# Performance work log

Hardware: AMD Instinct MI355X
Metric: run time of the kernel (lower is better)

The kernel has to match this reference:

```python
import jax, jax.numpy as jnp
import numpy as np

D_MODEL = 768
NUM_HEADS = 12
HEAD_DIM = D_MODEL // NUM_HEADS
B, T = 2, 4096


def setup_inputs() -> dict:
    key = jax.random.key(0)
    k1, k2, k3, k4, k5 = jax.random.split(key, 5)
    s_in = 1.0 / np.sqrt(D_MODEL)
    return {
        "x": jax.random.normal(k1, (B, T, D_MODEL), dtype=jnp.float32),
        "w_qkv": jax.random.normal(k2, (3 * D_MODEL, D_MODEL), dtype=jnp.float32) * s_in,
        "b_qkv": jax.random.normal(k3, (3 * D_MODEL,), dtype=jnp.float32) * 0.01,
        "w_out": jax.random.normal(k4, (D_MODEL, D_MODEL), dtype=jnp.float32) * s_in,
        "b_out": jax.random.normal(k5, (D_MODEL,), dtype=jnp.float32) * 0.01,
    }


def reference(x, w_qkv, b_qkv, w_out, b_out):
    b, t, c = x.shape
    # qkv: [B,T,3C] -> [3,B,H,T,Dh]  (torch Linear: x @ W.T + b)
    qkv = (x @ w_qkv.T + b_qkv).reshape(b, t, 3, NUM_HEADS, HEAD_DIM)
    qkv = jnp.transpose(qkv, (2, 0, 3, 1, 4))
    q, k, v = qkv[0], qkv[1], qkv[2]
    scale = 1.0 / np.sqrt(HEAD_DIM)
    scores = jnp.einsum("bhqd,bhkd->bhqk", q, k) * scale  # [B,H,T,T]
    causal = jnp.tril(jnp.ones((t, t), dtype=bool))
    scores = jnp.where(causal, scores, -jnp.inf)
    weights = jax.nn.softmax(scores, axis=-1)
    out = jnp.einsum("bhqk,bhkd->bhqd", weights, v)  # [B,H,T,Dh]
    out = jnp.transpose(out, (0, 2, 1, 3)).reshape(b, t, c)
    return out @ w_out.T + b_out
```

## Files before the change

kernel.cpp:

```cpp
#include <hip/hip_runtime.h>


#define NHEADS 12
#define DHEAD  64
#define TSEQ   4096
#define BATCH  2
#define CMODEL 768
#define MTOT   (BATCH * TSEQ)
#define NQKV   (3 * CMODEL)
#define NBH    (BATCH * NHEADS)

typedef __attribute__((ext_vector_type(8))) short s16x8;
typedef __attribute__((ext_vector_type(4))) float f32x4;
typedef __attribute__((ext_vector_type(4))) unsigned short u16x4;
typedef __attribute__((ext_vector_type(2))) unsigned int u32x2;

__device__ __forceinline__ unsigned short f2bf(float f) {
    unsigned u = __builtin_bit_cast(unsigned, f);
    u += 0x7fffu + ((u >> 16) & 1u);
    return (unsigned short)(u >> 16);
}

__device__ __forceinline__ unsigned pk2bf(float a, float b) {
    return (unsigned)f2bf(a) | ((unsigned)f2bf(b) << 16);
}

__device__ __forceinline__ unsigned cvtpk(float lo, float hi) {
    unsigned r;
    asm("v_cvt_pk_bf16_f32 %0, %1, %2" : "=v"(r) : "v"(lo), "v"(hi));
    return r;
}

__device__ __forceinline__ float fexp2(float x) {
    return __builtin_amdgcn_exp2f(x);
}

__device__ __forceinline__ void async_load16(const void* g, void* l) {
    __builtin_amdgcn_global_load_lds(
        (const __attribute__((address_space(1))) unsigned*)g,
        (__attribute__((address_space(3))) unsigned*)l, 16, 0, 0);
}

__device__ __forceinline__ void raw_barrier() {
    __builtin_amdgcn_sched_barrier(0);
    __builtin_amdgcn_s_barrier();
    __builtin_amdgcn_sched_barrier(0);
}

__global__ __launch_bounds__(256) void cvt3_kernel(
    const float* __restrict__ s0, const float* __restrict__ s1,
    const float* __restrict__ s2,
    unsigned short* __restrict__ d0, unsigned short* __restrict__ d1,
    unsigned short* __restrict__ d2, int n0, int n1, int n2)
{
    int i = blockIdx.x * 256 + threadIdx.x;
    const float* s; unsigned short* d; int j;
    if (i < n0)                { s = s0; d = d0; j = i; }
    else if (i < n0 + n1)      { s = s1; d = d1; j = i - n0; }
    else if (i < n0 + n1 + n2) { s = s2; d = d2; j = i - n0 - n1; }
    else return;
    f32x4 v = ((const f32x4*)s)[j];
    u32x2 o;
    o.x = pk2bf(v.x, v.y);
    o.y = pk2bf(v.z, v.w);
    ((u32x2*)d)[j] = o;
}

__global__ __launch_bounds__(256) void gemm_qkv_kernel(
    const unsigned short* __restrict__ A,
    const unsigned short* __restrict__ Bw,
    const float* __restrict__ bias,
    unsigned short* __restrict__ Qb,
    unsigned short* __restrict__ Kb,
    unsigned short* __restrict__ Vt)
{
    __shared__ unsigned short sA[128][64];
    __shared__ unsigned short sB[128][64];
    const int idx = blockIdx.x + blockIdx.y * 18;
    const int lid = (idx & 7) * 144 + (idx >> 3);
    const int n0 = (lid % 18) * 128;
    const int m0 = (lid / 18) * 128;
    const int tid = threadIdx.x;
    const int l = tid & 63, g = l >> 4, l15 = l & 15;
    const int w = tid >> 6, wm = w & 1, wn = w >> 1;
    const int wbase = tid & 192;
    const int seg = n0 / 768;

    f32x4 acc[4][4];
#pragma unroll
    for (int a = 0; a < 4; a++)
#pragma unroll
        for (int b = 0; b < 4; b++) acc[a][b] = (f32x4){0.f, 0.f, 0.f, 0.f};

    if (seg < 2) {
        for (int k0 = 0; k0 < 768; k0 += 64) {
#pragma unroll
            for (int i = 0; i < 4; i++) {
                const int idx2 = i * 256 + tid;
                const int row = idx2 >> 3, pc = idx2 & 7;
                const int lc = pc ^ (row & 7);
                async_load16(&A[(size_t)(m0 + row) * 768 + k0 + lc * 8],
                             &sA[0][0] + (size_t)(i * 256 + wbase) * 8);
                async_load16(&Bw[(size_t)(n0 + row) * 768 + k0 + lc * 8],
                             &sB[0][0] + (size_t)(i * 256 + wbase) * 8);
            }
            __syncthreads();
#pragma unroll
            for (int ks = 0; ks < 2; ks++) {
                const int cc = ((ks * 4 + g) ^ (l15 & 7)) * 8;
                s16x8 af[4], bf[4];
#pragma unroll
                for (int mt = 0; mt < 4; mt++)
                    af[mt] = *(const s16x8*)&sA[wm * 64 + mt * 16 + l15][cc];
#pragma unroll
                for (int nt = 0; nt < 4; nt++)
                    bf[nt] = *(const s16x8*)&sB[wn * 64 + nt * 16 + l15][cc];
#pragma unroll
                for (int nt = 0; nt < 4; nt++)
#pragma unroll
                    for (int mt = 0; mt < 4; mt++)
                        acc[nt][mt] = __builtin_amdgcn_mfma_f32_16x16x32_bf16(
                            bf[nt], af[mt], acc[nt][mt], 0, 0, 0);
            }
            __syncthreads();
        }

        unsigned short* dst = (seg == 0) ? Qb : Kb;
        const float sc = (seg == 0) ? 0.18033688011f : 1.0f;
        const int hh = ((n0 - seg * 768) + wn * 64) >> 6;
#pragma unroll
        for (int nt = 0; nt < 4; nt++) {
            const int dh = nt * 16 + g * 4;
            const f32x4 bv4 = *(const f32x4*)&bias[n0 + wn * 64 + dh];
#pragma unroll
            for (int mt = 0; mt < 4; mt++) {
                const int m = m0 + wm * 64 + mt * 16 + l15;
                const int b = m >> 12, t = m & 4095;
                u32x2 pk;
                pk.x = pk2bf((acc[nt][mt][0] + bv4[0]) * sc,
                             (acc[nt][mt][1] + bv4[1]) * sc);
                pk.y = pk2bf((acc[nt][mt][2] + bv4[2]) * sc,
                             (acc[nt][mt][3] + bv4[3]) * sc);
                *(u32x2*)&dst[(((size_t)(b * NHEADS + hh) * TSEQ + t) << 6) + dh] = pk;
            }
        }
    } else {
        for (int k0 = 0; k0 < 768; k0 += 64) {
#pragma unroll
            for (int i = 0; i < 4; i++) {
                const int idx2 = i * 256 + tid;
                const int row = idx2 >> 3, pc = idx2 & 7;
                const int lc = pc ^ (row & 7);
                async_load16(&A[(size_t)(m0 + row) * 768 + k0 + lc * 8],
                             &sA[0][0] + (size_t)(i * 256 + wbase) * 8);
                async_load16(&Bw[(size_t)(n0 + row) * 768 + k0 + lc * 8],
                             &sB[0][0] + (size_t)(i * 256 + wbase) * 8);
            }
            __syncthreads();
#pragma unroll
            for (int ks = 0; ks < 2; ks++) {
                const int cc = ((ks * 4 + g) ^ (l15 & 7)) * 8;
                s16x8 af[4], bf[4];
#pragma unroll
                for (int mt = 0; mt < 4; mt++)
                    af[mt] = *(const s16x8*)&sA[wm * 64 + mt * 16 + l15][cc];
#pragma unroll
                for (int nt = 0; nt < 4; nt++)
                    bf[nt] = *(const s16x8*)&sB[wn * 64 + nt * 16 + l15][cc];
#pragma unroll
                for (int mt = 0; mt < 4; mt++)
#pragma unroll
                    for (int nt = 0; nt < 4; nt++)
                        acc[mt][nt] = __builtin_amdgcn_mfma_f32_16x16x32_bf16(
                            af[mt], bf[nt], acc[mt][nt], 0, 0, 0);
            }
            __syncthreads();
        }

#pragma unroll
        for (int nt = 0; nt < 4; nt++) {
            const int n = n0 + wn * 64 + nt * 16 + l15;
            const float bv = bias[n];
            const int hh = (n - 1536) >> 6;
            const int dh = n & 63;
#pragma unroll
            for (int mt = 0; mt < 4; mt++) {
                const int mg = m0 + wm * 64 + mt * 16 + g * 4;
                const int b = mg >> 12, t = mg & 4095;
                u32x2 pk;
                pk.x = pk2bf(acc[mt][nt][0] + bv, acc[mt][nt][1] + bv);
                pk.y = pk2bf(acc[mt][nt][2] + bv, acc[mt][nt][3] + bv);
                *(u32x2*)&Vt[((size_t)(b * NHEADS + hh) * DHEAD + dh) * TSEQ + t] = pk;
            }
        }
    }
}

__device__ __forceinline__ void process_tile(
    const unsigned short (&sKb)[64][64],
    const unsigned short (&sVb)[64][64],
    unsigned short (&sPTw)[2][16][64],
    const s16x8 (&qa)[2][2],
    f32x4 (&o)[2][4], f32x4 (&lac)[2],
    s16x8 vones, int kt, int qg0, bool mask, int g, int l15)
{
    const int xk = l15 & 7;
    const int qg1 = qg0 + 16;

    f32x4 st[2][4];
#pragma unroll
    for (int nt = 0; nt < 4; nt++) {
        st[0][nt] = (f32x4){0.f, 0.f, 0.f, 0.f};
        st[1][nt] = (f32x4){0.f, 0.f, 0.f, 0.f};
    }
    __builtin_amdgcn_s_setprio(1);
#pragma unroll
    for (int ks = 0; ks < 2; ks++) {
        const int cc = ((ks * 4 + g) ^ xk) * 8;
#pragma unroll
        for (int nt = 0; nt < 4; nt++) {
            const s16x8 akf = *(const s16x8*)&sKb[nt * 16 + l15][cc];
            st[0][nt] = __builtin_amdgcn_mfma_f32_16x16x32_bf16(
                akf, qa[0][ks], st[0][nt], 0, 0, 0);
            st[1][nt] = __builtin_amdgcn_mfma_f32_16x16x32_bf16(
                akf, qa[1][ks], st[1][nt], 0, 0, 0);
        }
    }
    __builtin_amdgcn_s_setprio(0);

    if (mask) {
#pragma unroll
        for (int nt = 0; nt < 4; nt++)
#pragma unroll
            for (int r = 0; r < 4; r++) {
                const int key = kt + nt * 16 + g * 4 + r;
                if (key > qg0) st[0][nt][r] = -1e30f;
                if (key > qg1) st[1][nt][r] = -1e30f;
            }
    }

#pragma unroll
    for (int qf = 0; qf < 2; qf++) {
#pragma unroll
        for (int nt = 0; nt < 4; nt++) {
            float p0 = fexp2(st[qf][nt][0]);
            float p1 = fexp2(st[qf][nt][1]);
            float p2 = fexp2(st[qf][nt][2]);
            float p3 = fexp2(st[qf][nt][3]);
            u32x2 pk;
            pk.x = cvtpk(p0, p1);
            pk.y = cvtpk(p2, p3);
            const int phys = ((nt * 2 + (g >> 1)) ^ xk) * 8 + (g & 1) * 4;
            *(u32x2*)&sPTw[qf][l15][phys] = pk;
        }
    }

    __builtin_amdgcn_s_setprio(1);
#pragma unroll
    for (int ks = 0; ks < 2; ks++) {
        const int cc = ((ks * 4 + g) ^ xk) * 8;
        const s16x8 bp0 = *(const s16x8*)&sPTw[0][l15][cc];
        const s16x8 bp1 = *(const s16x8*)&sPTw[1][l15][cc];
#pragma unroll
        for (int nt = 0; nt < 4; nt++) {
            const s16x8 avf = *(const s16x8*)&sVb[nt * 16 + l15][cc];
            o[0][nt] = __builtin_amdgcn_mfma_f32_16x16x32_bf16(
                avf, bp0, o[0][nt], 0, 0, 0);
            o[1][nt] = __builtin_amdgcn_mfma_f32_16x16x32_bf16(
                avf, bp1, o[1][nt], 0, 0, 0);
        }
        lac[0] = __builtin_amdgcn_mfma_f32_16x16x32_bf16(vones, bp0, lac[0], 0, 0, 0);
        lac[1] = __builtin_amdgcn_mfma_f32_16x16x32_bf16(vones, bp1, lac[1], 0, 0, 0);
    }
    __builtin_amdgcn_s_setprio(0);
}

__global__ __launch_bounds__(256, 3) void attn_kernel(
    const unsigned short* __restrict__ Qb,
    const unsigned short* __restrict__ Kb,
    const unsigned short* __restrict__ Vt,
    unsigned short* __restrict__ Ob,
    float* __restrict__ oPart,
    float* __restrict__ lPart)
{
    __shared__ unsigned short sK[2][64][64];
    __shared__ unsigned short sV[2][64][64];
    __shared__ unsigned short sPT[4][2][16][64];
    const int bh   = blockIdx.x;
    const int p    = blockIdx.y >> 1;
    const int half = blockIdx.y & 1;
    const int jA = p, jB = 31 - p;
    const int nA = 2 * p + 2;
    const int aCount = (half == 0) ? nA : 0;
    const int bStart = (half == 0) ? 0 : (31 - 2 * p);
    const int bCount = 33 - aCount;
    const int tid = threadIdx.x;
    const int w = tid >> 6, l = tid & 63, g = l >> 4, l15 = l & 15;
    const int wbase = tid & 192;

    const int rl0 = w * 32 + l15;
    const int b = bh / NHEADS, hd = bh - b * NHEADS;

    s16x8 vones;
#pragma unroll
    for (int e = 0; e < 8; e++) vones[e] = (short)0x3F80;

    const unsigned short* Kbase = Kb + (size_t)bh * TSEQ * DHEAD;
    const unsigned short* Vbase = Vt + (size_t)bh * DHEAD * TSEQ;

    auto stage = [&](int jt, int buf) {
        const int kt = jt * 64;
#pragma unroll
        for (int pp = 0; pp < 2; pp++) {
            const int idx = pp * 256 + tid;
            const int row = idx >> 3, pc = idx & 7;
            const int lc = pc ^ (row & 7);
            async_load16(&Kbase[(size_t)(kt + row) * DHEAD + lc * 8],
                         &sK[buf][0][0] + (size_t)(pp * 256 + wbase) * 8);
            async_load16(&Vbase[(size_t)row * TSEQ + kt + lc * 8],
                         &sV[buf][0][0] + (size_t)(pp * 256 + wbase) * 8);
        }
    };

    stage((half == 0) ? 0 : bStart, 0);
    __syncthreads();

    if (half == 0) {
        const int qg0A = jA * 128 + rl0;
        const unsigned short* QpA = Qb + ((size_t)bh * TSEQ + qg0A) * DHEAD;
        s16x8 qA[2][2];
        qA[0][0] = *(const s16x8*)&QpA[g * 8];
        qA[0][1] = *(const s16x8*)&QpA[32 + g * 8];
        qA[1][0] = *(const s16x8*)&QpA[16 * DHEAD + g * 8];
        qA[1][1] = *(const s16x8*)&QpA[16 * DHEAD + 32 + g * 8];

        f32x4 oA[2][4];
        f32x4 lacA[2];
#pragma unroll
        for (int nt = 0; nt < 4; nt++) {
            oA[0][nt] = (f32x4){0.f, 0.f, 0.f, 0.f};
            oA[1][nt] = (f32x4){0.f, 0.f, 0.f, 0.f};
        }
        lacA[0] = (f32x4){0.f, 0.f, 0.f, 0.f};
        lacA[1] = (f32x4){0.f, 0.f, 0.f, 0.f};

        for (int s = 0; s < nA; s++) {
            const int buf = s & 1;
            if (s + 1 < nA) stage(s + 1, buf ^ 1);
            else stage(0, buf ^ 1);
            asm volatile("s_waitcnt vmcnt(4)" ::: "memory");
            process_tile(sK[buf], sV[buf], sPT[w], qA, oA, lacA, vones,
                         s * 64, qg0A, s >= nA - 2, g, l15);
            raw_barrier();
        }

#pragma unroll
        for (int qf = 0; qf < 2; qf++) {
            const int qg = qg0A + qf * 16;
            const float inv = 1.0f / lacA[qf][0];
#pragma unroll
            for (int nt = 0; nt < 4; nt++) {
                u32x2 pk;
                pk.x = pk2bf(oA[qf][nt][0] * inv, oA[qf][nt][1] * inv);
                pk.y = pk2bf(oA[qf][nt][2] * inv, oA[qf][nt][3] * inv);
                *(u32x2*)&Ob[((size_t)b * TSEQ + qg) * CMODEL + hd * DHEAD +
                             nt * 16 + g * 4] = pk;
            }
        }
    }

    {
        const int qg0B = jB * 128 + rl0;
        const unsigned short* QpB = Qb + ((size_t)bh * TSEQ + qg0B) * DHEAD;
        s16x8 qB[2][2];
        qB[0][0] = *(const s16x8*)&QpB[g * 8];
        qB[0][1] = *(const s16x8*)&QpB[32 + g * 8];
        qB[1][0] = *(const s16x8*)&QpB[16 * DHEAD + g * 8];
        qB[1][1] = *(const s16x8*)&QpB[16 * DHEAD + 32 + g * 8];

        f32x4 oB[2][4];
        f32x4 lacB[2];
#pragma unroll
        for (int nt = 0; nt < 4; nt++) {
            oB[0][nt] = (f32x4){0.f, 0.f, 0.f, 0.f};
            oB[1][nt] = (f32x4){0.f, 0.f, 0.f, 0.f};
        }
        lacB[0] = (f32x4){0.f, 0.f, 0.f, 0.f};
        lacB[1] = (f32x4){0.f, 0.f, 0.f, 0.f};

        for (int s = 0; s < bCount; s++) {
            const int buf = (aCount + s) & 1;
            if (s + 1 < bCount) {
                stage(bStart + s + 1, buf ^ 1);
                asm volatile("s_waitcnt vmcnt(4)" ::: "memory");
            } else {
                asm volatile("s_waitcnt vmcnt(0)" ::: "memory");
            }
            const bool mask = (half == 1) && (s >= 31);
            process_tile(sK[buf], sV[buf], sPT[w], qB, oB, lacB, vones,
                         (bStart + s) * 64, qg0B, mask, g, l15);
            raw_barrier();
        }

        const int pairIdx = bh * 16 + p;
        const size_t slot = (size_t)pairIdx * 2 + half;
        float* oS = oPart + slot * (128 * 64);
        float* lS = lPart + slot * 128;
#pragma unroll
        for (int qf = 0; qf < 2; qf++) {
            const int rl = rl0 + qf * 16;
#pragma unroll
            for (int nt = 0; nt < 4; nt++)
                *(f32x4*)&oS[(size_t)rl * 64 + nt * 16 + g * 4] = oB[qf][nt];
            if (g == 0) lS[rl] = lacB[qf][0];
        }
    }
}

__global__ __launch_bounds__(256) void combine_kernel(
    const float* __restrict__ oPart,
    const float* __restrict__ lPart,
    unsigned short* __restrict__ Ob)
{
    const int i = blockIdx.x * 256 + threadIdx.x;
    const int c4 = i & 15;
    const int rl = (i >> 4) & 127;
    const int p  = (i >> 11) & 15;
    const int bh = i >> 15;
    const int pair = bh * 16 + p;
    const float* o0 = oPart + ((size_t)pair * 2 + 0) * (128 * 64);
    const float* o1 = oPart + ((size_t)pair * 2 + 1) * (128 * 64);
    const float l0 = lPart[((size_t)pair * 2 + 0) * 128 + rl];
    const float l1 = lPart[((size_t)pair * 2 + 1) * 128 + rl];
    const float inv = 1.0f / (l0 + l1);
    const f32x4 a = *(const f32x4*)&o0[(size_t)rl * 64 + c4 * 4];
    const f32x4 c = *(const f32x4*)&o1[(size_t)rl * 64 + c4 * 4];
    const int b = bh / NHEADS, h = bh - b * NHEADS;
    const int qg = (31 - p) * 128 + rl;
    u32x2 pk;
    pk.x = pk2bf((a[0] + c[0]) * inv, (a[1] + c[1]) * inv);
    pk.y = pk2bf((a[2] + c[2]) * inv, (a[3] + c[3]) * inv);
    *(u32x2*)&Ob[((size_t)b * TSEQ + qg) * CMODEL + h * DHEAD + c4 * 4] = pk;
}

__global__ __launch_bounds__(256) void gemm_out_kernel(
    const unsigned short* __restrict__ A,
    const unsigned short* __restrict__ Bw,
    const float* __restrict__ bias,
    float* __restrict__ out)
{
    __shared__ unsigned short sA[128][64];
    __shared__ unsigned short sB[128][64];
    const int idx = blockIdx.x + blockIdx.y * 6;
    const int lid = (idx & 7) * 48 + (idx >> 3);
    const int n0 = (lid % 6) * 128;
    const int m0 = (lid / 6) * 128;
    const int tid = threadIdx.x;
    const int l = tid & 63, g = l >> 4, l15 = l & 15;
    const int w = tid >> 6, wm = w & 1, wn = w >> 1;
    const int wbase = tid & 192;

    f32x4 acc[4][4];
#pragma unroll
    for (int mt = 0; mt < 4; mt++)
#pragma unroll
        for (int nt = 0; nt < 4; nt++) acc[mt][nt] = (f32x4){0.f, 0.f, 0.f, 0.f};

    for (int k0 = 0; k0 < 768; k0 += 64) {
#pragma unroll
        for (int i = 0; i < 4; i++) {
            const int idx2 = i * 256 + tid;
            const int row = idx2 >> 3, pc = idx2 & 7;
            const int lc = pc ^ (row & 7);
            async_load16(&A[(size_t)(m0 + row) * 768 + k0 + lc * 8],
                         &sA[0][0] + (size_t)(i * 256 + wbase) * 8);
            async_load16(&Bw[(size_t)(n0 + row) * 768 + k0 + lc * 8],
                         &sB[0][0] + (size_t)(i * 256 + wbase) * 8);
        }
        __syncthreads();
#pragma unroll
        for (int ks = 0; ks < 2; ks++) {
            const int cc = ((ks * 4 + g) ^ (l15 & 7)) * 8;
            s16x8 af[4], bf[4];
#pragma unroll
            for (int mt = 0; mt < 4; mt++)
                af[mt] = *(const s16x8*)&sA[wm * 64 + mt * 16 + l15][cc];
#pragma unroll
            for (int nt = 0; nt < 4; nt++)
                bf[nt] = *(const s16x8*)&sB[wn * 64 + nt * 16 + l15][cc];
#pragma unroll
            for (int mt = 0; mt < 4; mt++)
#pragma unroll
                for (int nt = 0; nt < 4; nt++)
                    acc[mt][nt] = __builtin_amdgcn_mfma_f32_16x16x32_bf16(
                        af[mt], bf[nt], acc[mt][nt], 0, 0, 0);
        }
        __syncthreads();
    }

#pragma unroll
    for (int nt = 0; nt < 4; nt++) {
        const int n = n0 + wn * 64 + nt * 16 + l15;
        const float bv = bias[n];
#pragma unroll
        for (int mt = 0; mt < 4; mt++)
#pragma unroll
            for (int r = 0; r < 4; r++) {
                const int m = m0 + wm * 64 + mt * 16 + g * 4 + r;
                out[(size_t)m * CMODEL + n] = acc[mt][nt][r] + bv;
            }
    }
}

extern "C" void kernel_launch(void* const* d_in, const int* in_sizes, int n_in,
                              void* d_out, int out_size, void* d_ws, size_t ws_size,
                              hipStream_t stream) {
    const float* x     = (const float*)d_in[0];
    const float* w_qkv = (const float*)d_in[1];
    const float* b_qkv = (const float*)d_in[2];
    const float* w_out = (const float*)d_in[3];
    const float* b_out = (const float*)d_in[4];
    float* out = (float*)d_out;

    char* ws = (char*)d_ws;
    size_t off = 0;
    auto alloc = [&](size_t bytes) -> void* {
        void* p = (void*)(ws + off);
        off += (bytes + 255) & ~(size_t)255;
        return p;
    };
    unsigned short* xb    = (unsigned short*)alloc((size_t)MTOT * CMODEL * 2);
    unsigned short* wqkvb = (unsigned short*)alloc((size_t)NQKV * CMODEL * 2);
    unsigned short* woutb = (unsigned short*)alloc((size_t)CMODEL * CMODEL * 2);
    unsigned short* Qb    = (unsigned short*)alloc((size_t)NBH * TSEQ * DHEAD * 2);
    unsigned short* Kb    = (unsigned short*)alloc((size_t)NBH * TSEQ * DHEAD * 2);
    unsigned short* Vt    = (unsigned short*)alloc((size_t)NBH * TSEQ * DHEAD * 2);
    unsigned short* Ob    = (unsigned short*)alloc((size_t)MTOT * CMODEL * 2);
    float* oPart = (float*)alloc((size_t)NBH * 16 * 2 * 128 * 64 * 4);
    float* lPart = (float*)alloc((size_t)NBH * 16 * 2 * 128 * 4);

    const int n40 = MTOT * CMODEL / 4;
    const int n41 = NQKV * CMODEL / 4;
    const int n42 = CMODEL * CMODEL / 4;
    const int nblk = (n40 + n41 + n42 + 255) / 256;
    cvt3_kernel<<<dim3(nblk), 256, 0, stream>>>(
        x, w_qkv, w_out, xb, wqkvb, woutb, n40, n41, n42);

    gemm_qkv_kernel<<<dim3(NQKV / 128, MTOT / 128), 256, 0, stream>>>(
        xb, wqkvb, b_qkv, Qb, Kb, Vt);
    attn_kernel<<<dim3(NBH, 32), 256, 0, stream>>>(
        Qb, Kb, Vt, Ob, oPart, lPart);
    combine_kernel<<<dim3(NBH * 16 * 128 * 16 / 256), 256, 0, stream>>>(
        oPart, lPart, Ob);
    gemm_out_kernel<<<dim3(CMODEL / 128, MTOT / 128), 256, 0, stream>>>(
        Ob, woutb, b_out, out);
}
```

Measured before the change: 228.5 us.

## Use 2 waves per attention block with 64 query rows each, reusing K/V fragments

Attention blocks shrink from 4 waves to 2 waves, and each wave now handles 64 query rows (4 fragments) instead of 32. K and V fragments are loaded from shared memory into registers once per tile and reused across all four query fragments, which cuts LDS read traffic per FLOP. Staging loops are widened so 128 threads still fill the tiles, and the waitcnt thresholds are adjusted to match. The cost is much higher register pressure (launch bounds 128,2) and fewer waves per block to hide latency, with the P tile double-buffered by qf parity in the same wave.

```diff
diff --git a/kernel.cpp b/kernel.cpp
--- a/kernel.cpp
+++ b/kernel.cpp
@@ -196,86 +196,80 @@
     }
 }
 
-__device__ __forceinline__ void process_tile(
+__device__ __forceinline__ void process_tile4(
     const unsigned short (&sKb)[64][64],
     const unsigned short (&sVb)[64][64],
     unsigned short (&sPTw)[2][16][64],
-    const s16x8 (&qa)[2][2],
-    f32x4 (&o)[2][4], f32x4 (&lac)[2],
+    const s16x8 (&qa)[4][2],
+    f32x4 (&o)[4][4], f32x4 (&lac)[4],
     s16x8 vones, int kt, int qg0, bool mask, int g, int l15)
 {
     const int xk = l15 & 7;
-    const int qg1 = qg0 + 16;
-
-    f32x4 st[2][4];
-#pragma unroll
-    for (int nt = 0; nt < 4; nt++) {
-        st[0][nt] = (f32x4){0.f, 0.f, 0.f, 0.f};
-        st[1][nt] = (f32x4){0.f, 0.f, 0.f, 0.f};
-    }
-    __builtin_amdgcn_s_setprio(1);
+
+    s16x8 ak[2][4], av[2][4];
 #pragma unroll
     for (int ks = 0; ks < 2; ks++) {
         const int cc = ((ks * 4 + g) ^ xk) * 8;
 #pragma unroll
         for (int nt = 0; nt < 4; nt++) {
-            const s16x8 akf = *(const s16x8*)&sKb[nt * 16 + l15][cc];
-            st[0][nt] = __builtin_amdgcn_mfma_f32_16x16x32_bf16(
-                akf, qa[0][ks], st[0][nt], 0, 0, 0);
-            st[1][nt] = __builtin_amdgcn_mfma_f32_16x16x32_bf16(
-                akf, qa[1][ks], st[1][nt], 0, 0, 0);
-        }
-    }
-    __builtin_amdgcn_s_setprio(0);
-
-    if (mask) {
-#pragma unroll
-        for (int nt = 0; nt < 4; nt++)
-#pragma unroll
-            for (int r = 0; r < 4; r++) {
-                const int key = kt + nt * 16 + g * 4 + r;
-                if (key > qg0) st[0][nt][r] = -1e30f;
-                if (key > qg1) st[1][nt][r] = -1e30f;
-            }
-    }
-
-#pragma unroll
-    for (int qf = 0; qf < 2; qf++) {
+            ak[ks][nt] = *(const s16x8*)&sKb[nt * 16 + l15][cc];
+            av[ks][nt] = *(const s16x8*)&sVb[nt * 16 + l15][cc];
+        }
+    }
+
+#pragma unroll
+    for (int qf = 0; qf < 4; qf++) {
+        f32x4 st[4];
+#pragma unroll
+        for (int nt = 0; nt < 4; nt++) st[nt] = (f32x4){0.f, 0.f, 0.f, 0.f};
+        __builtin_amdgcn_s_setprio(1);
+#pragma unroll
+        for (int ks = 0; ks < 2; ks++)
+#pragma unroll
+            for (int nt = 0; nt < 4; nt++)
+                st[nt] = __builtin_amdgcn_mfma_f32_16x16x32_bf16(
+                    ak[ks][nt], qa[qf][ks], st[nt], 0, 0, 0);
+        __builtin_amdgcn_s_setprio(0);
+
+        if (mask) {
+            const int qg = qg0 + qf * 16;
+#pragma unroll
+            for (int nt = 0; nt < 4; nt++)
+#pragma unroll
+                for (int r = 0; r < 4; r++)
+                    if (kt + nt * 16 + g * 4 + r > qg) st[nt][r] = -1e30f;
+        }
+
 #pragma unroll
         for (int nt = 0; nt < 4; nt++) {
-            float p0 = fexp2(st[qf][nt][0]);
-            float p1 = fexp2(st[qf][nt][1]);
-            float p2 = fexp2(st[qf][nt][2]);
-            float p3 = fexp2(st[qf][nt][3]);
+            float p0 = fexp2(st[nt][0]);
+            float p1 = fexp2(st[nt][1]);
+            float p2 = fexp2(st[nt][2]);
+            float p3 = fexp2(st[nt][3]);
             u32x2 pk;
             pk.x = cvtpk(p0, p1);
             pk.y = cvtpk(p2, p3);
             const int phys = ((nt * 2 + (g >> 1)) ^ xk) * 8 + (g & 1) * 4;
-            *(u32x2*)&sPTw[qf][l15][phys] = pk;
-        }
-    }
-
-    __builtin_amdgcn_s_setprio(1);
-#pragma unroll
-    for (int ks = 0; ks < 2; ks++) {
-        const int cc = ((ks * 4 + g) ^ xk) * 8;
-        const s16x8 bp0 = *(const s16x8*)&sPTw[0][l15][cc];
-        const s16x8 bp1 = *(const s16x8*)&sPTw[1][l15][cc];
-#pragma unroll
-        for (int nt = 0; nt < 4; nt++) {
-            const s16x8 avf = *(const s16x8*)&sVb[nt * 16 + l15][cc];
-            o[0][nt] = __builtin_amdgcn_mfma_f32_16x16x32_bf16(
-                avf, bp0, o[0][nt], 0, 0, 0);
-            o[1][nt] = __builtin_amdgcn_mfma_f32_16x16x32_bf16(
-                avf, bp1, o[1][nt], 0, 0, 0);
-        }
-        lac[0] = __builtin_amdgcn_mfma_f32_16x16x32_bf16(vones, bp0, lac[0], 0, 0, 0);
-        lac[1] = __builtin_amdgcn_mfma_f32_16x16x32_bf16(vones, bp1, lac[1], 0, 0, 0);
-    }
-    __builtin_amdgcn_s_setprio(0);
-}
-
-__global__ __launch_bounds__(256, 3) void attn_kernel(
+            *(u32x2*)&sPTw[qf & 1][l15][phys] = pk;
+        }
+
+        __builtin_amdgcn_s_setprio(1);
+#pragma unroll
+        for (int ks = 0; ks < 2; ks++) {
+            const int cc = ((ks * 4 + g) ^ xk) * 8;
+            const s16x8 bp = *(const s16x8*)&sPTw[qf & 1][l15][cc];
+#pragma unroll
+            for (int nt = 0; nt < 4; nt++)
+                o[qf][nt] = __builtin_amdgcn_mfma_f32_16x16x32_bf16(
+                    av[ks][nt], bp, o[qf][nt], 0, 0, 0);
+            lac[qf] = __builtin_amdgcn_mfma_f32_16x16x32_bf16(
+                vones, bp, lac[qf], 0, 0, 0);
+        }
+        __builtin_amdgcn_s_setprio(0);
+    }
+}
+
+__global__ __launch_bounds__(128, 2) void attn_kernel(
     const unsigned short* __restrict__ Qb,
     const unsigned short* __restrict__ Kb,
     const unsigned short* __restrict__ Vt,
@@ -285,7 +279,7 @@
 {
     __shared__ unsigned short sK[2][64][64];
     __shared__ unsigned short sV[2][64][64];
-    __shared__ unsigned short sPT[4][2][16][64];
+    __shared__ unsigned short sPT[2][2][16][64];
     const int bh   = blockIdx.x;
     const int p    = blockIdx.y >> 1;
     const int half = blockIdx.y & 1;
@@ -296,9 +290,9 @@
     const int bCount = 33 - aCount;
     const int tid = threadIdx.x;
     const int w = tid >> 6, l = tid & 63, g = l >> 4, l15 = l & 15;
-    const int wbase = tid & 192;
-
-    const int rl0 = w * 32 + l15;
+    const int wbase = tid & 64;
+
+    const int rl0 = w * 64 + l15;
     const int b = bh / NHEADS, hd = bh - b * NHEADS;
 
     s16x8 vones;
@@ -311,14 +305,14 @@
     auto stage = [&](int jt, int buf) {
         const int kt = jt * 64;
 #pragma unroll
-        for (int pp = 0; pp < 2; pp++) {
-            const int idx = pp * 256 + tid;
+        for (int pp = 0; pp < 4; pp++) {
+            const int idx = pp * 128 + tid;
             const int row = idx >> 3, pc = idx & 7;
             const int lc = pc ^ (row & 7);
             async_load16(&Kbase[(size_t)(kt + row) * DHEAD + lc * 8],
-                         &sK[buf][0][0] + (size_t)(pp * 256 + wbase) * 8);
+                         &sK[buf][0][0] + (size_t)(pp * 128 + wbase) * 8);
             async_load16(&Vbase[(size_t)row * TSEQ + kt + lc * 8],
-                         &sV[buf][0][0] + (size_t)(pp * 256 + wbase) * 8);
+                         &sV[buf][0][0] + (size_t)(pp * 128 + wbase) * 8);
         }
     };
 
@@ -328,34 +322,35 @@
     if (half == 0) {
         const int qg0A = jA * 128 + rl0;
         const unsigned short* QpA = Qb + ((size_t)bh * TSEQ + qg0A) * DHEAD;
-        s16x8 qA[2][2];
-        qA[0][0] = *(const s16x8*)&QpA[g * 8];
-        qA[0][1] = *(const s16x8*)&QpA[32 + g * 8];
-        qA[1][0] = *(const s16x8*)&QpA[16 * DHEAD + g * 8];
-        qA[1][1] = *(const s16x8*)&QpA[16 * DHEAD + 32 + g * 8];
-
-        f32x4 oA[2][4];
-        f32x4 lacA[2];
-#pragma unroll
-        for (int nt = 0; nt < 4; nt++) {
-            oA[0][nt] = (f32x4){0.f, 0.f, 0.f, 0.f};
-            oA[1][nt] = (f32x4){0.f, 0.f, 0.f, 0.f};
-        }
-        lacA[0] = (f32x4){0.f, 0.f, 0.f, 0.f};
-        lacA[1] = (f32x4){0.f, 0.f, 0.f, 0.f};
+        s16x8 qA[4][2];
+#pragma unroll
+        for (int qf = 0; qf < 4; qf++) {
+            qA[qf][0] = *(const s16x8*)&QpA[(size_t)qf * 16 * DHEAD + g * 8];
+            qA[qf][1] = *(const s16x8*)&QpA[(size_t)qf * 16 * DHEAD + 32 + g * 8];
+        }
+
+        f32x4 oA[4][4];
+        f32x4 lacA[4];
+#pragma unroll
+        for (int qf = 0; qf < 4; qf++) {
+            lacA[qf] = (f32x4){0.f, 0.f, 0.f, 0.f};
+#pragma unroll
+            for (int nt = 0; nt < 4; nt++)
+                oA[qf][nt] = (f32x4){0.f, 0.f, 0.f, 0.f};
+        }
 
         for (int s = 0; s < nA; s++) {
             const int buf = s & 1;
             if (s + 1 < nA) stage(s + 1, buf ^ 1);
             else stage(0, buf ^ 1);
-            asm volatile("s_waitcnt vmcnt(4)" ::: "memory");
-            process_tile(sK[buf], sV[buf], sPT[w], qA, oA, lacA, vones,
-                         s * 64, qg0A, s >= nA - 2, g, l15);
+            asm volatile("s_waitcnt vmcnt(8)" ::: "memory");
+            process_tile4(sK[buf], sV[buf], sPT[w], qA, oA, lacA, vones,
+                          s * 64, qg0A, s >= nA - 2, g, l15);
             raw_barrier();
         }
 
 #pragma unroll
-        for (int qf = 0; qf < 2; qf++) {
+        for (int qf = 0; qf < 4; qf++) {
             const int qg = qg0A + qf * 16;
             const float inv = 1.0f / lacA[qf][0];
 #pragma unroll
@@ -372,33 +367,34 @@
     {
         const int qg0B = jB * 128 + rl0;
         const unsigned short* QpB = Qb + ((size_t)bh * TSEQ + qg0B) * DHEAD;
-        s16x8 qB[2][2];
-        qB[0][0] = *(const s16x8*)&QpB[g * 8];
-        qB[0][1] = *(const s16x8*)&QpB[32 + g * 8];
-        qB[1][0] = *(const s16x8*)&QpB[16 * DHEAD + g * 8];
-        qB[1][1] = *(const s16x8*)&QpB[16 * DHEAD + 32 + g * 8];
-
-        f32x4 oB[2][4];
-        f32x4 lacB[2];
-#pragma unroll
-        for (int nt = 0; nt < 4; nt++) {
-            oB[0][nt] = (f32x4){0.f, 0.f, 0.f, 0.f};
-            oB[1][nt] = (f32x4){0.f, 0.f, 0.f, 0.f};
-        }
-        lacB[0] = (f32x4){0.f, 0.f, 0.f, 0.f};
-        lacB[1] = (f32x4){0.f, 0.f, 0.f, 0.f};
+        s16x8 qB[4][2];
+#pragma unroll
+        for (int qf = 0; qf < 4; qf++) {
+            qB[qf][0] = *(const s16x8*)&QpB[(size_t)qf * 16 * DHEAD + g * 8];
+            qB[qf][1] = *(const s16x8*)&QpB[(size_t)qf * 16 * DHEAD + 32 + g * 8];
+        }
+
+        f32x4 oB[4][4];
+        f32x4 lacB[4];
+#pragma unroll
+        for (int qf = 0; qf < 4; qf++) {
+            lacB[qf] = (f32x4){0.f, 0.f, 0.f, 0.f};
+#pragma unroll
+            for (int nt = 0; nt < 4; nt++)
+                oB[qf][nt] = (f32x4){0.f, 0.f, 0.f, 0.f};
+        }
 
         for (int s = 0; s < bCount; s++) {
             const int buf = (aCount + s) & 1;
             if (s + 1 < bCount) {
                 stage(bStart + s + 1, buf ^ 1);
-                asm volatile("s_waitcnt vmcnt(4)" ::: "memory");
+                asm volatile("s_waitcnt vmcnt(8)" ::: "memory");
             } else {
                 asm volatile("s_waitcnt vmcnt(0)" ::: "memory");
             }
             const bool mask = (half == 1) && (s >= 31);
-            process_tile(sK[buf], sV[buf], sPT[w], qB, oB, lacB, vones,
-                         (bStart + s) * 64, qg0B, mask, g, l15);
+            process_tile4(sK[buf], sV[buf], sPT[w], qB, oB, lacB, vones,
+                          (bStart + s) * 64, qg0B, mask, g, l15);
             raw_barrier();
         }
 
@@ -407,7 +403,7 @@
         float* oS = oPart + slot * (128 * 64);
         float* lS = lPart + slot * 128;
 #pragma unroll
-        for (int qf = 0; qf < 2; qf++) {
+        for (int qf = 0; qf < 4; qf++) {
             const int rl = rl0 + qf * 16;
 #pragma unroll
             for (int nt = 0; nt < 4; nt++)
@@ -548,7 +544,7 @@
 
     gemm_qkv_kernel<<<dim3(NQKV / 128, MTOT / 128), 256, 0, stream>>>(
         xb, wqkvb, b_qkv, Qb, Kb, Vt);
-    attn_kernel<<<dim3(NBH, 32), 256, 0, stream>>>(
+    attn_kernel<<<dim3(NBH, 32), 128, 0, stream>>>(
         Qb, Kb, Vt, Ob, oPart, lPart);
     combine_kernel<<<dim3(NBH * 16 * 128 * 16 / 256), 256, 0, stream>>>(
         oPart, lPart, Ob);
```

Result: slower. 249.5 us (+9.2%).
